# Performance work log

Measured on AMD Instinct MI355X. Metric: run time of the kernel, lower is better.

## Reference

```python
import jax, jax.numpy as jnp
import numpy as np
import math

EMBED = 256
HEADS = 8
HD = EMBED // HEADS  # 32
NB = 3               # n_behaviors
C = NB * NB + 1      # 10 behavior-pair classes
NUM_BUCKETS = 32
MAX_DIST = 40
EPS = 1e-12
B, L = 4, 512


def _rel_bucket(seq_len, num_buckets=NUM_BUCKETS, max_distance=MAX_DIST):
    """T5-style relative position buckets, matching RelativePositionBias._relative_position_bucket."""
    pos = jnp.arange(seq_len)
    relative_position = pos[None, :] - pos[:, None]  # k - q
    n = -relative_position
    nb = num_buckets // 2
    ret = (n < 0).astype(jnp.int32) * nb
    n = jnp.abs(n)
    max_exact = nb // 2
    is_small = n < max_exact
    nf = jnp.maximum(n, 1).astype(jnp.float32)  # clamp to avoid log(0); masked by is_small anyway
    val_large = max_exact + (jnp.log(nf / max_exact) / math.log(max_distance / max_exact) * (nb - max_exact)).astype(jnp.int32)
    val_large = jnp.minimum(val_large, nb - 1)
    return ret + jnp.where(is_small, n, val_large)


def setup_inputs() -> dict:
    key = jax.random.key(0)
    ks = jax.random.split(key, 12)
    s = 0.02
    return {
        "input_tensor": jax.random.normal(ks[0], (B, L, EMBED), jnp.float32),
        "attention_mask": jnp.zeros((B, 1, L, L), jnp.float32),
        "type_seq": jax.random.randint(ks[1], (B, L), 0, NB + 1),
        "Wq": jax.random.normal(ks[2], (NB + 1, EMBED, HEADS, HD), jnp.float32) * s,
        "Wk": jax.random.normal(ks[3], (NB + 1, EMBED, HEADS, HD), jnp.float32) * s,
        "Wv": jax.random.normal(ks[4], (NB + 1, EMBED, HEADS, HD), jnp.float32) * s,
        "W1": jax.random.normal(ks[5], (NB, HEADS, HD, HD), jnp.float32) * s,
        "alpha1": jax.random.normal(ks[6], (C, NB, HEADS), jnp.float32),
        "W2": jax.random.normal(ks[7], (NB, HEADS, HD, HD), jnp.float32) * s,
        "alpha2": jax.random.normal(ks[8], (C, NB, HEADS), jnp.float32),
        "rp_tables": jax.random.normal(ks[9], (C, NUM_BUCKETS, HEADS), jnp.float32) * s,
        "ln_gamma": jnp.ones((EMBED,), jnp.float32),
        "ln_beta": jnp.zeros((EMBED,), jnp.float32),
    }


def reference(input_tensor, attention_mask, type_seq, Wq, Wk, Wv, W1, alpha1, W2, alpha2, rp_tables, ln_gamma, ln_beta):
    bsz, seq_len, emb = input_tensor.shape
    ts = type_seq
    # behavior pair matrix: 0 if either side is padding, else (tq-1)*NB + tk in [1, NB^2]
    bm = ((ts[:, :, None] * ts[:, None, :]) != 0).astype(jnp.int32)
    bm = bm * ((ts[:, :, None] - 1) * NB + ts[:, None, :])  # [B,L,L]

    # --- relative position bias, gathered per behavior pair ---
    bucket = _rel_bucket(seq_len)                 # [L,L]
    vals = rp_tables[:, bucket, :]                # [C,L,L,H]
    qi = jnp.arange(seq_len)[None, :, None]
    ki = jnp.arange(seq_len)[None, None, :]
    bias = vals[bm, qi, ki]                       # [B,L,L,H] gathered along C per pair
    bias = jnp.transpose(bias, (0, 3, 1, 2))      # [B,H,L,L]

    # --- behavior-gated QKV ---
    oh = jax.nn.one_hot(ts, NB + 1, dtype=input_tensor.dtype)  # [B,L,NB+1]
    q = jnp.einsum('BLH,bHhd,BLb->BhLd', input_tensor, Wq, oh)
    k = jnp.einsum('BLH,bHhd,BLb->BhLd', input_tensor, Wk, oh)
    v = jnp.einsum('BLH,bHhd,BLb->BhLd', input_tensor, Wv, oh)

    # --- bilinear scores with per-pair mixing matrices ---
    W1_ = jnp.einsum('bhmn,Cbh->Chmn', W1, jax.nn.softmax(alpha1, axis=1))
    att_all = jnp.einsum('BhQm,Chmn,BhKn->BhQKC', q, W1_, k)  # [B,H,L,L,C]
    scores = jnp.take_along_axis(att_all, bm[:, None, :, :, None], axis=4)[..., 0]
    scores = scores * (1.0 / math.sqrt(HD)) + bias + attention_mask
    probs = jax.nn.softmax(scores, axis=-1)  # dropout=0.0 -> identity

    # --- behavior-mixed value aggregation ---
    W2_ = jnp.einsum('bhmn,Cbh->Chmn', W2, jax.nn.softmax(alpha2, axis=1))
    oh_bm = jax.nn.one_hot(bm, C, dtype=probs.dtype)          # [B,L,L,C]
    pC = probs[:, :, :, :, None] * oh_bm[:, None]             # [B,H,L,L,C]
    ctx = jnp.einsum('BhQKC,Chnm,BhKn->BhQm', pC, W2_, v)     # [B,H,L,d]

    ctx = jnp.transpose(ctx, (0, 2, 1, 3)).reshape(bsz, seq_len, emb)
    x = ctx + input_tensor  # out_dropout=0.0
    mu = jnp.mean(x, axis=-1, keepdims=True)
    var = jnp.mean(jnp.square(x - mu), axis=-1, keepdims=True)
    return (x - mu) / jnp.sqrt(var + EPS) * ln_gamma + ln_beta
```

## Files before the change

### kernel.cpp

```cpp
#include <hip/hip_runtime.h>
#include <math.h>

#define BB 4
#define LL 512
#define EMB 256
#define NH 8
#define HD 32
#define NB_ 3
#define CCN 10
#define NBKT 32
#define SCALE 0.17677669529663687f

typedef __bf16 bf16_t;
typedef __attribute__((ext_vector_type(8))) bf16_t bf16x8;
typedef __attribute__((ext_vector_type(4))) float f32x4;

__device__ __forceinline__ unsigned short f2b(float f) {
    unsigned int u = __float_as_uint(f);
    u += 0x7FFF + ((u >> 16) & 1);
    return (unsigned short)(u >> 16);
}
__device__ __forceinline__ float b2f(unsigned short s) {
    return __uint_as_float(((unsigned int)s) << 16);
}
__device__ __forceinline__ unsigned pack2(float a, float b) {
    return (unsigned)f2b(a) | ((unsigned)f2b(b) << 16);
}
__device__ __forceinline__ int bm_of(int tq, int tk) {
    return (tq * tk != 0) ? ((tq - 1) * 3 + tk) : 0;
}
__device__ __forceinline__ unsigned long long shfl_up64(unsigned long long v, int d) {
    unsigned lo = (unsigned)__shfl_up((int)(unsigned)v, d, 64);
    unsigned hi = (unsigned)__shfl_up((int)(v >> 32), d, 64);
    return (((unsigned long long)hi) << 32) | lo;
}

__device__ __forceinline__ void sort512(const int* __restrict__ tsb, int* spk,
                                        unsigned long long* wtll, int* msc, int tid) {
    int ty0 = tsb[2 * tid], ty1 = tsb[2 * tid + 1];
    unsigned long long pk = (1ULL << (16 * ty0)) + (1ULL << (16 * ty1));
    unsigned long long v = pk;
    int lane = tid & 63;
#pragma unroll
    for (int off = 1; off < 64; off <<= 1) {
        unsigned long long o = shfl_up64(v, off);
        if (lane >= off) v += o;
    }
    int w = tid >> 6;
    if (lane == 63) wtll[w] = v;
    __syncthreads();
    unsigned long long pre = 0, tot = 0;
#pragma unroll
    for (int i = 0; i < 4; i++) {
        unsigned long long xx = wtll[i];
        if (i < w) pre += xx;
        tot += xx;
    }
    v += pre;
    unsigned long long excl = v - pk;
    int c0 = (int)(tot & 0xFFFF), c1 = (int)((tot >> 16) & 0xFFFF);
    int c2 = (int)((tot >> 32) & 0xFFFF), c3 = (int)((tot >> 48) & 0xFFFF);
    int ub0 = 0, ub1 = c0, ub2 = c0 + c1, ub3 = c0 + c1 + c2;
    if (tid == 0) {
        int pc0 = (c0 + 31) & ~31, pc1 = (c1 + 31) & ~31, pc2 = (c2 + 31) & ~31, pc3 = (c3 + 31) & ~31;
        int pb1 = pc0, pb2 = pc0 + pc1, pb3 = pc0 + pc1 + pc2;
        msc[0] = 0;  msc[1] = pb1; msc[2] = pb2; msc[3] = pb3;
        msc[4] = ub0; msc[5] = ub1; msc[6] = ub2; msc[7] = ub3;
        msc[8] = c0; msc[9] = c1; msc[10] = c2; msc[11] = c3;
        msc[12] = (pb3 + pc3 + 63) & ~63;
    }
    int bases[4] = {ub0, ub1, ub2, ub3};
    int r0 = (int)((excl >> (16 * ty0)) & 0xFFFF);
    unsigned long long excl1 = excl + (1ULL << (16 * ty0));
    int r1 = (int)((excl1 >> (16 * ty1)) & 0xFFFF);
    spk[bases[ty0] + r0] = (ty0 << 16) | (2 * tid);
    spk[bases[ty1] + r1] = (ty1 << 16) | (2 * tid + 1);
    __syncthreads();
}

__device__ __forceinline__ void pad_lookup(const int* msc, int pos, int& real, int& upos, int& seg) {
    seg = (pos >= msc[1]) + (pos >= msc[2]) + (pos >= msc[3]);
    int r = pos - msc[seg];
    real = (r < msc[8 + seg]) ? 1 : 0;
    upos = msc[4 + seg] + r;
}

__global__ void k_pre(const float* __restrict__ A1, const float* __restrict__ W1,
                      const float* __restrict__ A2, const float* __restrict__ W2,
                      const float* __restrict__ Wq, const float* __restrict__ Wk, const float* __restrict__ Wv,
                      const float* __restrict__ am,
                      float* __restrict__ W1s, float* __restrict__ W2s,
                      unsigned short* __restrict__ W1Tb, unsigned short* __restrict__ W2Tb,
                      unsigned short* __restrict__ Wt, int* __restrict__ mflag) {
    __shared__ float cmb[32 * 33];
    __shared__ unsigned short ls[64 * 264];
    int g = blockIdx.x, tid = threadIdx.x;
    if (g < 160) {
        int idx = g;
        const float* alpha = (idx < 80) ? A1 : A2;
        const float* W     = (idx < 80) ? W1 : W2;
        float* Ws          = (idx < 80) ? W1s : W2s;
        unsigned short* WT = (idx < 80) ? W1Tb : W2Tb;
        idx %= 80;
        int cc = idx / NH, h = idx % NH;
        float a0 = alpha[cc * NB_ * NH + 0 * NH + h];
        float a1 = alpha[cc * NB_ * NH + 1 * NH + h];
        float a2 = alpha[cc * NB_ * NH + 2 * NH + h];
        float mx = fmaxf(a0, fmaxf(a1, a2));
        float e0 = __expf(a0 - mx), e1 = __expf(a1 - mx), e2 = __expf(a2 - mx);
        float inv = 1.0f / (e0 + e1 + e2);
        e0 *= inv; e1 *= inv; e2 *= inv;
        for (int i = tid; i < HD * HD; i += 256) {
            int m = i >> 5, n = i & 31;
            float acc = e0 * W[((0 * NH + h) * HD + m) * HD + n]
                      + e1 * W[((1 * NH + h) * HD + m) * HD + n]
                      + e2 * W[((2 * NH + h) * HD + m) * HD + n];
            cmb[m * 33 + n] = acc;
        }
        __syncthreads();
        for (int i = tid; i < HD * HD; i += 256) {
            int a = i >> 5, bq = i & 31;
            Ws[((cc * NH + h) * HD + a) * HD + bq] = cmb[a * 33 + bq];
            WT[((size_t)(cc * NH + h) * HD + a) * HD + bq] = f2b(cmb[bq * 33 + a]);
        }
        return;
    }
    if (g < 208) {
        int t = g - 160;
        int tw = t >> 2, ob = t & 3;
        int which = tw >> 2, ty = tw & 3;
        const float* src = ((which == 0) ? Wq : (which == 1) ? Wk : Wv) + (size_t)ty * EMB * EMB;
        int out0 = ob * 64;
        for (int it = 0; it < 16; it++) {
            int e = it * 16 + (tid >> 4);
            int o4 = (tid & 15) * 4;
            float4 v = *(const float4*)&src[(size_t)e * EMB + out0 + o4];
            ls[(o4 + 0) * 264 + e] = f2b(v.x);
            ls[(o4 + 1) * 264 + e] = f2b(v.y);
            ls[(o4 + 2) * 264 + e] = f2b(v.z);
            ls[(o4 + 3) * 264 + e] = f2b(v.w);
        }
        __syncthreads();
        int out = tid >> 2, ech = (tid & 3) * 8;
        unsigned short* dst = Wt + (size_t)tw * EMB * EMB + (size_t)(out0 + out) * EMB;
        const unsigned short* srcl = &ls[out * 264];
#pragma unroll
        for (int jj = 0; jj < 8; jj++)
            *(uint4*)&dst[ech + jj * 32] = *(const uint4*)&srcl[ech + jj * 32];
        return;
    }
    {
        int idx = g - 208;
        const uint4* p = (const uint4*)am + (size_t)idx * 1024;
        unsigned o = 0;
#pragma unroll
        for (int j = 0; j < 4; j++) {
            uint4 v = p[tid + j * 256];
            o |= v.x | v.y | v.z | v.w;
        }
        if (o) atomicOr(mflag, 1);
    }
}

__global__ __launch_bounds__(256, 4) void k_qkv(
    const float* __restrict__ x, const int* __restrict__ ts,
    const unsigned short* __restrict__ Wt,
    unsigned short* __restrict__ qp, unsigned short* __restrict__ kp, unsigned short* __restrict__ vp) {
    __shared__ int spk[LL];
    __shared__ unsigned long long wtll[4];
    __shared__ int msc[16];

    int g = blockIdx.x, tid = threadIdx.x;
    int ns = g % 6, gb = g / 6;
    int b = gb >> 4, tb = gb & 15, i0 = tb * 32;
    int which = ns >> 1, nh = ns & 1;
    int wave = tid >> 6, lane = tid & 63, quad = lane >> 4, col = lane & 15;

    sort512(ts + b * LL, spk, wtll, msc, tid);

    bf16x8 afr[2][8];
#pragma unroll
    for (int mt = 0; mt < 2; mt++) {
        int orig = spk[i0 + mt * 16 + col] & 0xFFFF;
        const float* xr = &x[(size_t)(b * LL + orig) * EMB];
#pragma unroll
        for (int kc = 0; kc < 8; kc++) {
            float4 v0 = *(const float4*)&xr[kc * 32 + quad * 8];
            float4 v1 = *(const float4*)&xr[kc * 32 + quad * 8 + 4];
            uint4 up;
            up.x = pack2(v0.x, v0.y); up.y = pack2(v0.z, v0.w);
            up.z = pack2(v1.x, v1.y); up.w = pack2(v1.z, v1.w);
            afr[mt][kc] = *(bf16x8*)&up;
        }
    }
    int t_start = spk[i0] >> 16, t_end = spk[i0 + 31] >> 16;
    unsigned short* outp = (which == 0) ? qp : (which == 1) ? kp : vp;

    for (int ty = t_start; ty <= t_end; ty++) {
        f32x4 acc[2][2];
#pragma unroll
        for (int mt = 0; mt < 2; mt++)
#pragma unroll
            for (int nt = 0; nt < 2; nt++) acc[mt][nt] = (f32x4){0.f, 0.f, 0.f, 0.f};
        const unsigned short* wsrc = Wt + (size_t)(which * 4 + ty) * EMB * EMB + (size_t)(nh * 128) * EMB;
        const unsigned short* w0 = &wsrc[(size_t)((wave * 2 + 0) * 16 + col) * EMB + quad * 8];
        const unsigned short* w1 = &wsrc[(size_t)((wave * 2 + 1) * 16 + col) * EMB + quad * 8];
#pragma unroll
        for (int kc = 0; kc < 8; kc++) {
            bf16x8 b0 = *(const bf16x8*)&w0[kc * 32];
            bf16x8 b1 = *(const bf16x8*)&w1[kc * 32];
            acc[0][0] = __builtin_amdgcn_mfma_f32_16x16x32_bf16(afr[0][kc], b0, acc[0][0], 0, 0, 0);
            acc[0][1] = __builtin_amdgcn_mfma_f32_16x16x32_bf16(afr[0][kc], b1, acc[0][1], 0, 0, 0);
            acc[1][0] = __builtin_amdgcn_mfma_f32_16x16x32_bf16(afr[1][kc], b0, acc[1][0], 0, 0, 0);
            acc[1][1] = __builtin_amdgcn_mfma_f32_16x16x32_bf16(afr[1][kc], b1, acc[1][1], 0, 0, 0);
        }
#pragma unroll
        for (int mt = 0; mt < 2; mt++)
#pragma unroll
            for (int r = 0; r < 4; r++) {
                int tokloc = mt * 16 + quad * 4 + r;
                int tty = spk[i0 + tokloc] >> 16;
                if (tty != ty) continue;
#pragma unroll
                for (int nt = 0; nt < 2; nt++) {
                    int n = nh * 128 + (wave * 2 + nt) * 16 + col;
                    int h = n >> 5, d = n & 31;
                    outp[((size_t)(b * NH + h) * LL + i0 + tokloc) * HD + d] = f2b(acc[mt][nt][r]);
                }
            }
    }
}

#define SCP 648
#define OFF_UN   20736
#define OFF_QTB  29184
#define OFF_KPAD 33536
#define OFF_TBL  36096
#define OFF_RPL  37120
#define OFF_WT   38400
#define OFF_QOR  38432
#define OFF_QTY  38496
#define OFF_INV  38560
#define OFF_MSC  38624
#define SM_TOTAL 38688
__global__ __launch_bounds__(256, 4) void k_attn(
    const unsigned short* __restrict__ qp, const unsigned short* __restrict__ kp,
    const unsigned short* __restrict__ vp,
    const int* __restrict__ ts, const float* __restrict__ rp, const float* __restrict__ am,
    const float* __restrict__ W1s, const float* __restrict__ W2s,
    const unsigned short* __restrict__ W1Tb, const unsigned short* __restrict__ W2Tb,
    const int* __restrict__ mflag, float* __restrict__ ctx) {
    __shared__ __align__(16) char smem[SM_TOTAL];
    unsigned short* scu = (unsigned short*)smem;
    int*   spk  = (int*)smem;
    unsigned short* qstb = (unsigned short*)(smem + OFF_UN);
    unsigned short* vt   = (unsigned short*)(smem + OFF_UN);
    float* sb   = (float*)(smem + OFF_UN);
    unsigned short* qtb = (unsigned short*)(smem + OFF_QTB);
    unsigned short* sbb = (unsigned short*)(smem + OFF_QTB);
    int*   kpad = (int*)(smem + OFF_KPAD);
    short* tbl  = (short*)(smem + OFF_TBL);
    float* rp_l = (float*)(smem + OFF_RPL);
    unsigned long long* wtll = (unsigned long long*)(smem + OFF_WT);
    int*   qor_l = (int*)(smem + OFF_QOR);
    int*   qty_l = (int*)(smem + OFF_QTY);
    float* inv_l = (float*)(smem + OFF_INV);
    int*   msc   = (int*)(smem + OFF_MSC);

    int blk = blockIdx.x;
    int b = blk >> 8, h = (blk >> 5) & 7, q16 = blk & 31;
    int i0q = q16 * 16;
    int tid = threadIdx.x;
    int wave = tid >> 6, lane = tid & 63, quad = lane >> 4, col = lane & 15;
    int bh = b * NH + h;
    int mz = (mflag[0] == 0);

    for (int d = tid; d < LL; d += 256) {
        int v;
        if (d < 8) v = d;
        else {
            double r = log((double)d / 8.0) / log(5.0);
            v = 8 + (int)(r * 8.0);
            if (v > 15) v = 15;
        }
        tbl[d] = (short)v;
    }
    for (int i = tid; i < CCN * NBKT; i += 256) rp_l[i] = rp[i * NH + h];

    sort512(ts + b * LL, spk, wtll, msc, tid);

    int KT = msc[12];
    if (tid < 16) {
        int v = spk[i0q + tid];
        qor_l[tid] = v & 0xFFFF; qty_l[tid] = v >> 16;
    }
    for (int pos = tid; pos < KT; pos += 256) {
        int real, upos, seg;
        pad_lookup(msc, pos, real, upos, seg);
        int orig = real ? (spk[upos] & 0xFFFF) : 0x3FF;
        kpad[pos] = (seg << 20) | ((real ? upos : 0) << 10) | orig;
    }
    {
        int q = tid >> 4, m2 = (tid & 15) * 2;
        ((unsigned*)qstb)[q * 20 + (tid & 15)] =
            *(const unsigned*)&qp[((size_t)bh * LL + i0q + q) * HD + m2];
    }
    __syncthreads();

    int qor_r[4], qty_r[4];
#pragma unroll
    for (int r = 0; r < 4; r++) { qor_r[r] = qor_l[quad * 4 + r]; qty_r[r] = qty_l[quad * 4 + r]; }
    bool uniq = (qty_l[0] == qty_l[15]);
    int tqu = qty_l[0];

    if (uniq) {
#pragma unroll
        for (int it = 0; it < 2; it++) {
            int t8 = wave * 2 + it;
            int tk = t8 >> 1, nhf = t8 & 1;
            int bmv = bm_of(tqu, tk);
            bf16x8 a = *(const bf16x8*)&qstb[col * 40 + quad * 8];
            bf16x8 bb = *(const bf16x8*)&W1Tb[((size_t)(bmv * NH + h) * HD + nhf * 16 + col) * HD + quad * 8];
            f32x4 d = {0.f, 0.f, 0.f, 0.f};
            d = __builtin_amdgcn_mfma_f32_16x16x32_bf16(a, bb, d, 0, 0, 0);
#pragma unroll
            for (int r = 0; r < 4; r++)
                qtb[(quad * 4 + r) * 136 + tk * 32 + nhf * 16 + col] = f2b(d[r]);
        }
    } else {
        for (int i = tid; i < 16 * 128; i += 256) {
            int q = i >> 7, r = i & 127, tk = r >> 5, n = r & 31;
            int bmv = bm_of(qty_l[q], tk);
            const float* wb = &W1s[((bmv * NH + h) * HD) * HD + n];
            float acc = 0.f;
#pragma unroll
            for (int m = 0; m < HD; m++) acc += b2f(qstb[q * 40 + m]) * wb[m * HD];
            qtb[q * 136 + tk * 32 + n] = f2b(acc);
        }
    }
    __syncthreads();

    const float* amb = am + (size_t)b * LL * LL;
    int ntiles = KT >> 4;
    for (int tile = wave; tile < ntiles; tile += 4) {
        int kb = tile * 16;
        int kv0 = kpad[kb];
        if ((kv0 & 0x3FF) == 0x3FF) {
#pragma unroll
            for (int r = 0; r < 4; r++) scu[(quad * 4 + r) * SCP + kb + col] = 0xFF80;
            continue;
        }
        int tkt = kv0 >> 20;
        int kpi = kb + col;
        int kv = kpad[kpi];
        int ko = kv & 0x3FF;
        int upos = (kv >> 10) & 0x3FF;
        bool real = (ko != 0x3FF);
        bf16x8 bfr;
        if (real) bfr = *(const bf16x8*)&kp[((size_t)bh * LL + upos) * HD + quad * 8];
        else { uint4 z = make_uint4(0, 0, 0, 0); bfr = *(bf16x8*)&z; }
        bf16x8 a = *(const bf16x8*)&qtb[col * 136 + tkt * 32 + quad * 8];
        f32x4 d = {0.f, 0.f, 0.f, 0.f};
        d = __builtin_amdgcn_mfma_f32_16x16x32_bf16(a, bfr, d, 0, 0, 0);
        if (!real) {
#pragma unroll
            for (int r = 0; r < 4; r++) scu[(quad * 4 + r) * SCP + kpi] = 0xFF80;
        } else {
#pragma unroll
            for (int r = 0; r < 4; r++) {
                int q = quad * 4 + r;
                int qo = qor_r[r];
                int dd = qo - ko;
                int ad = dd < 0 ? -dd : dd;
                int bk = (dd < 0 ? 16 : 0) + (int)tbl[ad];
                float sv = d[r] * SCALE + rp_l[bm_of(qty_r[r], tkt) * NBKT + bk];
                if (!mz) sv += amb[(size_t)qo * LL + ko];
                scu[q * SCP + kpi] = f2b(sv);
            }
        }
    }
    __syncthreads();

    {
        int gq = tid >> 4, t16 = tid & 15;
        float mx = -1e30f;
        for (int kk = t16; kk < KT; kk += 16) mx = fmaxf(mx, b2f(scu[gq * SCP + kk]));
#pragma unroll
        for (int off = 1; off < 16; off <<= 1) mx = fmaxf(mx, __shfl_xor(mx, off, 16));
        float sum = 0.f;
        for (int kk = t16; kk < KT; kk += 16) {
            int idx = gq * SCP + kk;
            float e = __expf(b2f(scu[idx]) - mx);
            scu[idx] = f2b(e); sum += e;
        }
#pragma unroll
        for (int off = 1; off < 16; off <<= 1) sum += __shfl_xor(sum, off, 16);
        if (t16 == 0) inv_l[gq] = 1.0f / sum;
    }
    __syncthreads();

    f32x4 accv[4][2];
#pragma unroll
    for (int t = 0; t < 4; t++)
#pragma unroll
        for (int hh = 0; hh < 2; hh++) accv[t][hh] = (f32x4){0.f, 0.f, 0.f, 0.f};

    for (int kt0 = 0; kt0 < KT; kt0 += 64) {
        {
            int kk = tid >> 2, n8 = (tid & 3) * 8;
            int kv = kpad[kt0 + kk];
            int upos = (kv >> 10) & 0x3FF;
            bool real = ((kv & 0x3FF) != 0x3FF);
            uint4 w = make_uint4(0, 0, 0, 0);
            if (real) w = *(const uint4*)&vp[((size_t)bh * LL + upos) * HD + n8];
            unsigned short sv[8] = {
                (unsigned short)(w.x & 0xFFFF), (unsigned short)(w.x >> 16),
                (unsigned short)(w.y & 0xFFFF), (unsigned short)(w.y >> 16),
                (unsigned short)(w.z & 0xFFFF), (unsigned short)(w.z >> 16),
                (unsigned short)(w.w & 0xFFFF), (unsigned short)(w.w >> 16)};
#pragma unroll
            for (int i = 0; i < 8; i++) {
                int n = n8 + i;
                int ph = ((n & 3) << 3) | (n >> 2);
                vt[ph * 72 + kk] = sv[i];
            }
        }
        __syncthreads();
        int c = kt0 >> 6;
        int g0 = 2 * c;
        int pc = ((col & 3) << 3) | (col >> 2);
#pragma unroll
        for (int gl = 0; gl < 2; gl++) {
            int gg = g0 + gl;
            if ((gg & 3) != wave) continue;
            int loc = gl * 32;
            int kvg = kpad[kt0 + loc];
            if ((kvg & 0x3FF) == 0x3FF) continue;
            int tk = kvg >> 20;
            bf16x8 a = *(const bf16x8*)&scu[col * SCP + kt0 + loc + quad * 8];
            bf16x8 b0 = *(const bf16x8*)&vt[pc * 72 + loc + quad * 8];
            bf16x8 b1 = *(const bf16x8*)&vt[(pc + 4) * 72 + loc + quad * 8];
            if (tk == 0) {
                accv[0][0] = __builtin_amdgcn_mfma_f32_16x16x32_bf16(a, b0, accv[0][0], 0, 0, 0);
                accv[0][1] = __builtin_amdgcn_mfma_f32_16x16x32_bf16(a, b1, accv[0][1], 0, 0, 0);
            } else if (tk == 1) {
                accv[1][0] = __builtin_amdgcn_mfma_f32_16x16x32_bf16(a, b0, accv[1][0], 0, 0, 0);
                accv[1][1] = __builtin_amdgcn_mfma_f32_16x16x32_bf16(a, b1, accv[1][1], 0, 0, 0);
            } else if (tk == 2) {
                accv[2][0] = __builtin_amdgcn_mfma_f32_16x16x32_bf16(a, b0, accv[2][0], 0, 0, 0);
                accv[2][1] = __builtin_amdgcn_mfma_f32_16x16x32_bf16(a, b1, accv[2][1], 0, 0, 0);
            } else {
                accv[3][0] = __builtin_amdgcn_mfma_f32_16x16x32_bf16(a, b0, accv[3][0], 0, 0, 0);
                accv[3][1] = __builtin_amdgcn_mfma_f32_16x16x32_bf16(a, b1, accv[3][1], 0, 0, 0);
            }
        }
        __syncthreads();
    }

#pragma unroll
    for (int w = 0; w < 4; w++) {
        if (wave == w) {
#pragma unroll
            for (int t = 0; t < 4; t++)
#pragma unroll
                for (int hh = 0; hh < 2; hh++)
#pragma unroll
                    for (int r = 0; r < 4; r++) {
                        int q = quad * 4 + r;
                        int n = col + 16 * hh;
                        float val = accv[t][hh][r];
                        if (w == 0) {
                            sb[q * 132 + t * 32 + n] = val;
                        } else if (w < 3) {
                            sb[q * 132 + t * 32 + n] += val;
                        } else {
                            float fin = sb[q * 132 + t * 32 + n] + val;
                            sb[q * 132 + t * 32 + n] = fin;
                            sbb[q * 136 + t * 32 + n] = f2b(fin);
                        }
                    }
        }
        __syncthreads();
    }

    if (uniq) {
        if (wave < 2) {
            int mhf = wave;
            f32x4 d = {0.f, 0.f, 0.f, 0.f};
#pragma unroll
            for (int tk = 0; tk < 4; tk++) {
                int bmv = bm_of(tqu, tk);
                bf16x8 a = *(const bf16x8*)&sbb[col * 136 + tk * 32 + quad * 8];
                bf16x8 bb = *(const bf16x8*)&W2Tb[((size_t)(bmv * NH + h) * HD + mhf * 16 + col) * HD + quad * 8];
                d = __builtin_amdgcn_mfma_f32_16x16x32_bf16(a, bb, d, 0, 0, 0);
            }
#pragma unroll
            for (int r = 0; r < 4; r++) {
                int q = quad * 4 + r;
                ctx[((size_t)(b * LL + qor_l[q])) * EMB + h * HD + mhf * 16 + col] = d[r] * inv_l[q];
            }
        }
    } else {
        int m = tid & 31, qq = tid >> 5;
#pragma unroll
        for (int rep = 0; rep < 2; rep++) {
            int qi = qq + 8 * rep;
            int tq = qty_l[qi];
            float acc = 0.f;
#pragma unroll
            for (int tk2 = 0; tk2 < 4; tk2++) {
                int bmv = bm_of(tq, tk2);
                const float* wb = &W2s[((bmv * NH + h) * HD) * HD + m];
                const float* sbp = &sb[qi * 132 + tk2 * 32];
                for (int n = 0; n < HD; n++) acc += sbp[n] * wb[n * HD];
            }
            int qo = qor_l[qi];
            ctx[((size_t)(b * LL + qo)) * EMB + h * HD + m] = acc * inv_l[qi];
        }
    }
}

__global__ void k_ln(const float* __restrict__ ctx, const float* __restrict__ x,
                     const float* __restrict__ gamma, const float* __restrict__ beta,
                     float* __restrict__ out) {
    __shared__ float red[8];
    __shared__ float red2[8];
    int blk = blockIdx.x;
    int b = blk >> 9, l = blk & 511;
    int j = threadIdx.x;
    size_t base = ((size_t)(b * LL + l)) * EMB;
    float v = ctx[base + j] + x[base + j];
    float s = v, s2 = v * v;
    for (int off = 32; off > 0; off >>= 1) { s += __shfl_down(s, off, 64); s2 += __shfl_down(s2, off, 64); }
    int wid = j >> 6;
    if ((j & 63) == 0) { red[wid] = s; red2[wid] = s2; }
    __syncthreads();
    if (j == 0) {
        float ts_ = 0, ts2 = 0;
        for (int w = 0; w < 4; w++) { ts_ += red[w]; ts2 += red2[w]; }
        red[4] = ts_; red2[4] = ts2;
    }
    __syncthreads();
    float mu = red[4] / (float)EMB;
    float var = red2[4] / (float)EMB - mu * mu;
    float r = rsqrtf(var + 1e-12f);
    out[base + j] = (v - mu) * r * gamma[j] + beta[j];
}

extern "C" void kernel_launch(void* const* d_in, const int* in_sizes, int n_in,
                              void* d_out, int out_size, void* d_ws, size_t ws_size,
                              hipStream_t stream) {
    const float* x  = (const float*)d_in[0];
    const float* am = (const float*)d_in[1];
    const int*   ts = (const int*)d_in[2];
    const float* Wq = (const float*)d_in[3];
    const float* Wk = (const float*)d_in[4];
    const float* Wv = (const float*)d_in[5];
    const float* W1 = (const float*)d_in[6];
    const float* a1 = (const float*)d_in[7];
    const float* W2 = (const float*)d_in[8];
    const float* a2 = (const float*)d_in[9];
    const float* rp = (const float*)d_in[10];
    const float* g  = (const float*)d_in[11];
    const float* be = (const float*)d_in[12];
    float* out = (float*)d_out;

    float* ws  = (float*)d_ws;
    float* W1s = ws;
    float* W2s = ws + 81920;
    unsigned short* W1Tb = (unsigned short*)(ws + 163840);
    unsigned short* W2Tb = (unsigned short*)(ws + 204800);
    int* mflag = (int*)(ws + 245760);
    unsigned short* qp = (unsigned short*)(ws + 245776);
    unsigned short* kp = qp + BB * NH * LL * HD;
    unsigned short* vp = kp + BB * NH * LL * HD;
    float* ctx = (float*)(vp + BB * NH * LL * HD);
    unsigned short* Wt = (unsigned short*)ctx;

    hipMemsetAsync(mflag, 0, 4, stream);
    hipLaunchKernelGGL(k_pre, dim3(464), dim3(256), 0, stream,
                       a1, W1, a2, W2, Wq, Wk, Wv, am, W1s, W2s, W1Tb, W2Tb, Wt, mflag);
    hipLaunchKernelGGL(k_qkv, dim3(384), dim3(256), 0, stream, x, ts, Wt, qp, kp, vp);
    hipLaunchKernelGGL(k_attn, dim3(BB * NH * 32), dim3(256), 0, stream,
                       qp, kp, vp, ts, rp, am, W1s, W2s, W1Tb, W2Tb, mflag, ctx);
    hipLaunchKernelGGL(k_ln, dim3(BB * LL), dim3(256), 0, stream, ctx, x, g, be, out);
}
```

Baseline: 144.6 us.

## Write V pre-transposed in padded key order and drop memset via per-block mask flags

The QKV kernel now writes V through a shared-memory transpose into a transposed, padded-key-order global buffer (vpT). The attention kernel can then feed MFMA B fragments straight from global memory, with no per-tile V staging in LDS and no __syncthreads inside the PV loop. The attention-mask flag becomes a per-block array written without atomics, which removes the hipMemsetAsync launch; each attention block reduces the 256 flags with a wave vote. The cost is extra syncs and scattered transposed stores in k_qkv, and uncached global loads in the attention inner loop.

```diff
diff --git a/kernel.cpp b/kernel.cpp
--- a/kernel.cpp
+++ b/kernel.cpp
@@ -91,9 +91,10 @@
                       const float* __restrict__ am,
                       float* __restrict__ W1s, float* __restrict__ W2s,
                       unsigned short* __restrict__ W1Tb, unsigned short* __restrict__ W2Tb,
-                      unsigned short* __restrict__ Wt, int* __restrict__ mflag) {
+                      unsigned short* __restrict__ Wt, int* __restrict__ mflagArr) {
     __shared__ float cmb[32 * 33];
     __shared__ unsigned short ls[64 * 264];
+    __shared__ int reds[4];
     int g = blockIdx.x, tid = threadIdx.x;
     if (g < 160) {
         int idx = g;
@@ -158,17 +159,22 @@
             uint4 v = p[tid + j * 256];
             o |= v.x | v.y | v.z | v.w;
         }
-        if (o) atomicOr(mflag, 1);
+        int wv = __any(o != 0);
+        if ((tid & 63) == 0) reds[tid >> 6] = wv;
+        __syncthreads();
+        if (tid == 0) mflagArr[idx] = reds[0] | reds[1] | reds[2] | reds[3];
     }
 }
 
 __global__ __launch_bounds__(256, 4) void k_qkv(
     const float* __restrict__ x, const int* __restrict__ ts,
     const unsigned short* __restrict__ Wt,
-    unsigned short* __restrict__ qp, unsigned short* __restrict__ kp, unsigned short* __restrict__ vp) {
+    unsigned short* __restrict__ qp, unsigned short* __restrict__ kp,
+    unsigned short* __restrict__ vpT) {
     __shared__ int spk[LL];
     __shared__ unsigned long long wtll[4];
     __shared__ int msc[16];
+    __shared__ unsigned short vt_l[128 * 33];
 
     int g = blockIdx.x, tid = threadIdx.x;
     int ns = g % 6, gb = g / 6;
@@ -194,7 +200,7 @@
         }
     }
     int t_start = spk[i0] >> 16, t_end = spk[i0 + 31] >> 16;
-    unsigned short* outp = (which == 0) ? qp : (which == 1) ? kp : vp;
+    unsigned short* outp = (which == 0) ? qp : kp;
 
     for (int ty = t_start; ty <= t_end; ty++) {
         f32x4 acc[2][2];
@@ -214,20 +220,45 @@
             acc[1][0] = __builtin_amdgcn_mfma_f32_16x16x32_bf16(afr[1][kc], b0, acc[1][0], 0, 0, 0);
             acc[1][1] = __builtin_amdgcn_mfma_f32_16x16x32_bf16(afr[1][kc], b1, acc[1][1], 0, 0, 0);
         }
-#pragma unroll
-        for (int mt = 0; mt < 2; mt++)
-#pragma unroll
-            for (int r = 0; r < 4; r++) {
-                int tokloc = mt * 16 + quad * 4 + r;
-                int tty = spk[i0 + tokloc] >> 16;
-                if (tty != ty) continue;
+        if (which < 2) {
+#pragma unroll
+            for (int mt = 0; mt < 2; mt++)
+#pragma unroll
+                for (int r = 0; r < 4; r++) {
+                    int tokloc = mt * 16 + quad * 4 + r;
+                    int tty = spk[i0 + tokloc] >> 16;
+                    if (tty != ty) continue;
+#pragma unroll
+                    for (int nt = 0; nt < 2; nt++) {
+                        int n = nh * 128 + (wave * 2 + nt) * 16 + col;
+                        int h = n >> 5, d = n & 31;
+                        outp[((size_t)(b * NH + h) * LL + i0 + tokloc) * HD + d] = f2b(acc[mt][nt][r]);
+                    }
+                }
+        } else {
+#pragma unroll
+            for (int mt = 0; mt < 2; mt++)
 #pragma unroll
                 for (int nt = 0; nt < 2; nt++) {
-                    int n = nh * 128 + (wave * 2 + nt) * 16 + col;
-                    int h = n >> 5, d = n & 31;
-                    outp[((size_t)(b * NH + h) * LL + i0 + tokloc) * HD + d] = f2b(acc[mt][nt][r]);
+                    int ln = (wave * 2 + nt) * 16 + col;
+#pragma unroll
+                    for (int r = 0; r < 4; r++)
+                        vt_l[ln * 33 + mt * 16 + quad * 4 + r] = f2b(acc[mt][nt][r]);
                 }
+            __syncthreads();
+            int ub = msc[4 + ty], cnt = msc[8 + ty], pb = msc[ty];
+            int lo = ub - i0; if (lo < 0) lo = 0;
+            int hi = ub + cnt - i0; if (hi > 32) hi = 32;
+            int run = hi - lo;
+            int pbase = pb + i0 + lo - ub;
+            int rowbase = b * 256 + nh * 128;
+            int t32 = tid & 31;
+            if (t32 < run) {
+                for (int rr = tid >> 5; rr < 128; rr += 8)
+                    vpT[(size_t)(rowbase + rr) * 640 + pbase + t32] = vt_l[rr * 33 + lo + t32];
             }
+            __syncthreads();
+        }
     }
 }
 
@@ -245,16 +276,16 @@
 #define SM_TOTAL 38688
 __global__ __launch_bounds__(256, 4) void k_attn(
     const unsigned short* __restrict__ qp, const unsigned short* __restrict__ kp,
-    const unsigned short* __restrict__ vp,
+    const unsigned short* __restrict__ vpT,
     const int* __restrict__ ts, const float* __restrict__ rp, const float* __restrict__ am,
     const float* __restrict__ W1s, const float* __restrict__ W2s,
     const unsigned short* __restrict__ W1Tb, const unsigned short* __restrict__ W2Tb,
-    const int* __restrict__ mflag, float* __restrict__ ctx) {
+    const int* __restrict__ mflagArr, float* __restrict__ ctx) {
     __shared__ __align__(16) char smem[SM_TOTAL];
+    __shared__ int msk_s;
     unsigned short* scu = (unsigned short*)smem;
     int*   spk  = (int*)smem;
     unsigned short* qstb = (unsigned short*)(smem + OFF_UN);
-    unsigned short* vt   = (unsigned short*)(smem + OFF_UN);
     float* sb   = (float*)(smem + OFF_UN);
     unsigned short* qtb = (unsigned short*)(smem + OFF_QTB);
     unsigned short* sbb = (unsigned short*)(smem + OFF_QTB);
@@ -273,8 +304,14 @@
     int tid = threadIdx.x;
     int wave = tid >> 6, lane = tid & 63, quad = lane >> 4, col = lane & 15;
     int bh = b * NH + h;
-    int mz = (mflag[0] == 0);
-
+
+    if (wave == 0) {
+        int v = 0;
+#pragma unroll
+        for (int j = 0; j < 4; j++) v |= mflagArr[lane + 64 * j];
+        int anyv = __any(v != 0);
+        if (lane == 0) msk_s = anyv;
+    }
     for (int d = tid; d < LL; d += 256) {
         int v;
         if (d < 8) v = d;
@@ -290,6 +327,7 @@
     sort512(ts + b * LL, spk, wtll, msc, tid);
 
     int KT = msc[12];
+    int mz = (msk_s == 0);
     if (tid < 16) {
         int v = spk[i0q + tid];
         qor_l[tid] = v & 0xFFFF; qty_l[tid] = v >> 16;
@@ -405,57 +443,31 @@
 #pragma unroll
         for (int hh = 0; hh < 2; hh++) accv[t][hh] = (f32x4){0.f, 0.f, 0.f, 0.f};
 
-    for (int kt0 = 0; kt0 < KT; kt0 += 64) {
-        {
-            int kk = tid >> 2, n8 = (tid & 3) * 8;
-            int kv = kpad[kt0 + kk];
-            int upos = (kv >> 10) & 0x3FF;
-            bool real = ((kv & 0x3FF) != 0x3FF);
-            uint4 w = make_uint4(0, 0, 0, 0);
-            if (real) w = *(const uint4*)&vp[((size_t)bh * LL + upos) * HD + n8];
-            unsigned short sv[8] = {
-                (unsigned short)(w.x & 0xFFFF), (unsigned short)(w.x >> 16),
-                (unsigned short)(w.y & 0xFFFF), (unsigned short)(w.y >> 16),
-                (unsigned short)(w.z & 0xFFFF), (unsigned short)(w.z >> 16),
-                (unsigned short)(w.w & 0xFFFF), (unsigned short)(w.w >> 16)};
-#pragma unroll
-            for (int i = 0; i < 8; i++) {
-                int n = n8 + i;
-                int ph = ((n & 3) << 3) | (n >> 2);
-                vt[ph * 72 + kk] = sv[i];
-            }
-        }
-        __syncthreads();
-        int c = kt0 >> 6;
-        int g0 = 2 * c;
-        int pc = ((col & 3) << 3) | (col >> 2);
-#pragma unroll
-        for (int gl = 0; gl < 2; gl++) {
-            int gg = g0 + gl;
-            if ((gg & 3) != wave) continue;
-            int loc = gl * 32;
-            int kvg = kpad[kt0 + loc];
-            if ((kvg & 0x3FF) == 0x3FF) continue;
-            int tk = kvg >> 20;
-            bf16x8 a = *(const bf16x8*)&scu[col * SCP + kt0 + loc + quad * 8];
-            bf16x8 b0 = *(const bf16x8*)&vt[pc * 72 + loc + quad * 8];
-            bf16x8 b1 = *(const bf16x8*)&vt[(pc + 4) * 72 + loc + quad * 8];
-            if (tk == 0) {
-                accv[0][0] = __builtin_amdgcn_mfma_f32_16x16x32_bf16(a, b0, accv[0][0], 0, 0, 0);
-                accv[0][1] = __builtin_amdgcn_mfma_f32_16x16x32_bf16(a, b1, accv[0][1], 0, 0, 0);
-            } else if (tk == 1) {
-                accv[1][0] = __builtin_amdgcn_mfma_f32_16x16x32_bf16(a, b0, accv[1][0], 0, 0, 0);
-                accv[1][1] = __builtin_amdgcn_mfma_f32_16x16x32_bf16(a, b1, accv[1][1], 0, 0, 0);
-            } else if (tk == 2) {
-                accv[2][0] = __builtin_amdgcn_mfma_f32_16x16x32_bf16(a, b0, accv[2][0], 0, 0, 0);
-                accv[2][1] = __builtin_amdgcn_mfma_f32_16x16x32_bf16(a, b1, accv[2][1], 0, 0, 0);
-            } else {
-                accv[3][0] = __builtin_amdgcn_mfma_f32_16x16x32_bf16(a, b0, accv[3][0], 0, 0, 0);
-                accv[3][1] = __builtin_amdgcn_mfma_f32_16x16x32_bf16(a, b1, accv[3][1], 0, 0, 0);
-            }
-        }
-        __syncthreads();
-    }
+    const unsigned short* vbase = &vpT[(size_t)(b * 256 + h * 32) * 640];
+    int ngroups = KT >> 5;
+    for (int gg = wave; gg < ngroups; gg += 4) {
+        int loc = gg << 5;
+        int kvg = kpad[loc];
+        if ((kvg & 0x3FF) == 0x3FF) continue;
+        int tk = kvg >> 20;
+        bf16x8 a = *(const bf16x8*)&scu[col * SCP + loc + quad * 8];
+        bf16x8 b0 = *(const bf16x8*)&vbase[(size_t)col * 640 + loc + quad * 8];
+        bf16x8 b1 = *(const bf16x8*)&vbase[(size_t)(col + 16) * 640 + loc + quad * 8];
+        if (tk == 0) {
+            accv[0][0] = __builtin_amdgcn_mfma_f32_16x16x32_bf16(a, b0, accv[0][0], 0, 0, 0);
+            accv[0][1] = __builtin_amdgcn_mfma_f32_16x16x32_bf16(a, b1, accv[0][1], 0, 0, 0);
+        } else if (tk == 1) {
+            accv[1][0] = __builtin_amdgcn_mfma_f32_16x16x32_bf16(a, b0, accv[1][0], 0, 0, 0);
+            accv[1][1] = __builtin_amdgcn_mfma_f32_16x16x32_bf16(a, b1, accv[1][1], 0, 0, 0);
+        } else if (tk == 2) {
+            accv[2][0] = __builtin_amdgcn_mfma_f32_16x16x32_bf16(a, b0, accv[2][0], 0, 0, 0);
+            accv[2][1] = __builtin_amdgcn_mfma_f32_16x16x32_bf16(a, b1, accv[2][1], 0, 0, 0);
+        } else {
+            accv[3][0] = __builtin_amdgcn_mfma_f32_16x16x32_bf16(a, b0, accv[3][0], 0, 0, 0);
+            accv[3][1] = __builtin_amdgcn_mfma_f32_16x16x32_bf16(a, b1, accv[3][1], 0, 0, 0);
+        }
+    }
+    __syncthreads();
 
 #pragma unroll
     for (int w = 0; w < 4; w++) {
@@ -570,18 +582,17 @@
     float* W2s = ws + 81920;
     unsigned short* W1Tb = (unsigned short*)(ws + 163840);
     unsigned short* W2Tb = (unsigned short*)(ws + 204800);
-    int* mflag = (int*)(ws + 245760);
-    unsigned short* qp = (unsigned short*)(ws + 245776);
+    int* mflagArr = (int*)(ws + 245760);
+    unsigned short* qp = (unsigned short*)(ws + 246016);
     unsigned short* kp = qp + BB * NH * LL * HD;
-    unsigned short* vp = kp + BB * NH * LL * HD;
-    float* ctx = (float*)(vp + BB * NH * LL * HD);
+    unsigned short* vpT = kp + BB * NH * LL * HD;
+    float* ctx = (float*)(vpT + BB * 256 * 640);
     unsigned short* Wt = (unsigned short*)ctx;
 
-    hipMemsetAsync(mflag, 0, 4, stream);
     hipLaunchKernelGGL(k_pre, dim3(464), dim3(256), 0, stream,
-                       a1, W1, a2, W2, Wq, Wk, Wv, am, W1s, W2s, W1Tb, W2Tb, Wt, mflag);
-    hipLaunchKernelGGL(k_qkv, dim3(384), dim3(256), 0, stream, x, ts, Wt, qp, kp, vp);
+                       a1, W1, a2, W2, Wq, Wk, Wv, am, W1s, W2s, W1Tb, W2Tb, Wt, mflagArr);
+    hipLaunchKernelGGL(k_qkv, dim3(384), dim3(256), 0, stream, x, ts, Wt, qp, kp, vpT);
     hipLaunchKernelGGL(k_attn, dim3(BB * NH * 32), dim3(256), 0, stream,
-                       qp, kp, vp, ts, rp, am, W1s, W2s, W1Tb, W2Tb, mflag, ctx);
+                       qp, kp, vpT, ts, rp, am, W1s, W2s, W1Tb, W2Tb, mflagArr, ctx);
     hipLaunchKernelGGL(k_ln, dim3(BB * LL), dim3(256), 0, stream, ctx, x, g, be, out);
 }
```

Result: faster. 140.7 us (-2.7%).
